# Kernel optimization log

Measured on AMD Instinct MI355X. Metric: run time of the kernel, lower is better.

Reference implementation:

```python
import jax, jax.numpy as jnp
import numpy as np

N_COARSE = 64  # n_coarse samples per ray
EPS = 1e-8
DELTA_INF = 1e10


def setup_inputs() -> dict:
    key = jax.random.key(0)
    ks = jax.random.split(key, 8)
    B, H = 16384, 256
    near = 2.0 + jax.random.uniform(ks[0], (B, 1), dtype=jnp.float32)
    far = 6.0 + jax.random.uniform(ks[1], (B, 1), dtype=jnp.float32)
    center = jax.random.normal(ks[2], (B, 3), dtype=jnp.float32)
    direction = jax.random.normal(ks[3], (B, 3), dtype=jnp.float32)
    direction = direction / jnp.linalg.norm(direction, axis=-1, keepdims=True)
    # stand-in NeRF field: 3 -> 256 -> 256 -> 4 MLP (rgb + sigma)
    W1 = jax.random.normal(ks[4], (3, H), dtype=jnp.float32) * 0.5
    b1 = jnp.zeros((H,), jnp.float32)
    W2 = jax.random.normal(ks[5], (H, H), dtype=jnp.float32) * (1.0 / np.sqrt(H))
    b2 = jnp.zeros((H,), jnp.float32)
    W3 = jax.random.normal(ks[6], (H, 4), dtype=jnp.float32) * (1.0 / np.sqrt(H))
    b3 = jnp.zeros((4,), jnp.float32)
    return {"near": near, "far": far, "center": center, "direction": direction,
            "W1": W1, "b1": b1, "W2": W2, "b2": b2, "W3": W3, "b3": b3}


def reference(near, far, center, direction, W1, b1, W2, b2, W3, b3):
    B = near.shape[0]
    K = N_COARSE
    # sample_coarse: stratified z values, lindisp=False, perturb=0
    z_steps = jnp.linspace(0.0, 1.0, K, dtype=near.dtype)[None, :]          # (1, K)
    z_vals = near * (1.0 - z_steps) + far * z_steps                          # (B, K)
    # composite(): deltas with infinite last interval
    deltas = jnp.concatenate(
        [z_vals[:, 1:] - z_vals[:, :-1],
         jnp.full((B, 1), DELTA_INF, dtype=z_vals.dtype)], axis=-1)          # (B, K)
    # world-space sample points along each ray
    points = center[:, None, :] + z_vals[:, :, None] * direction[:, None, :]  # (B, K, 3)
    # model(points) -> (B, K, 4): rgb + sigma
    h = jax.nn.relu(points @ W1 + b1)
    h = jax.nn.relu(h @ W2 + b2)
    out = h @ W3 + b3
    rgbs = out[..., :3]                                                      # (B, K, 3)
    sigmas = out[..., 3]                                                     # (B, K)
    sigmas_last = sigmas[:, -1]
    # alpha compositing (noise_std=0, training=False -> no noise)
    alphas = 1.0 - jnp.exp(-deltas * jax.nn.relu(sigmas))                    # (B, K)
    alphas_shifted = jnp.concatenate(
        [jnp.ones((B, 1), alphas.dtype), 1.0 - alphas + EPS], axis=-1)       # (B, K+1)
    T = jnp.cumprod(alphas_shifted, axis=-1)                                 # transmittance
    weights = alphas * T[:, :-1]                                             # (B, K)
    rgb_final = jnp.sum(weights[..., None] * rgbs, axis=-2)                  # (B, 3)
    depth_final = jnp.sum(weights * z_vals, axis=-1)                         # (B,)
    # white background: rgb += 1 - accumulated alpha
    pix_alpha = jnp.sum(weights, axis=1)
    rgb_final = rgb_final + 1.0 - pix_alpha[:, None]
    return rgb_final, depth_final, weights, sigmas_last
```

## Files before the change

### kernel.cpp

```cpp
#include <hip/hip_runtime.h>
#include <hip/hip_bf16.h>


constexpr int H  = 256;
constexpr int KS = 64;

typedef __attribute__((ext_vector_type(8))) short short8;
typedef __attribute__((ext_vector_type(4))) float f32x4;

__device__ __forceinline__ f32x4 mfma16(short8 a, short8 b, f32x4 c) {
    return __builtin_amdgcn_mfma_f32_16x16x32_bf16(a, b, c, 0, 0, 0);
}
__device__ __forceinline__ void split_bf16(float x, short& hi, short& lo) {
    __hip_bfloat16 h = __float2bfloat16(x);
    float hf = __bfloat162float(h);
    __hip_bfloat16 l = __float2bfloat16(x - hf);
    union { __hip_bfloat16 b; short s; } c1, c2;
    c1.b = h; c2.b = l;
    hi = c1.s; lo = c2.s;
}
__device__ __forceinline__ unsigned short f2bf(float x) {
    union { __hip_bfloat16 b; unsigned short s; } c;
    c.b = __float2bfloat16(x);
    return c.s;
}
__device__ __forceinline__ float bf2f(unsigned short s) {
    union { unsigned int u; float f; } c;
    c.u = ((unsigned int)s) << 16;
    return c.f;
}
__device__ __forceinline__ unsigned int pack2bf(float a, float b) {
    return (unsigned int)f2bf(a) | ((unsigned int)f2bf(b) << 16);
}

__global__ void pack_w2_kernel(const float* __restrict__ W2,
                               unsigned short* __restrict__ hi,
                               unsigned short* __restrict__ lo)
{
    const int i  = blockIdx.x * 256 + threadIdx.x;
    const int e  = i & 7;
    const int l  = (i >> 3) & 63;
    const int nt = (i >> 9) & 15;
    const int ks = i >> 13;
    const int k  = ks * 32 + (l >> 4) * 8 + e;
    const int n  = nt * 16 + (l & 15);
    short h, lw;
    split_bf16(W2[k * H + n], h, lw);
    hi[i] = (unsigned short)h;
    lo[i] = (unsigned short)lw;
}

struct SM {
    unsigned short A0[8 * 4 * 64 * 8];
    unsigned short A1[8 * 4 * 64 * 8];
    unsigned short L0[8 * 64 * 8];
    unsigned short L1[8 * 64 * 8];
};

#define PH1(nr_, fa_, cx_, cy_, cz_, dx_, dy_, dz_, Abuf, Lbuf)                  \
do {                                                                             \
    const int kbase = wv * 32 + (lane >> 4) * 8;                                 \
    float w1r[3][8], b1r[8];                                                     \
    _Pragma("unroll")                                                            \
    for (int c = 0; c < 3; ++c) {                                                \
        const f32x4 a_ = *(const f32x4*)&W1[c * H + kbase];                      \
        const f32x4 b_ = *(const f32x4*)&W1[c * H + kbase + 4];                  \
        _Pragma("unroll")                                                        \
        for (int e = 0; e < 4; ++e) { w1r[c][e] = a_[e]; w1r[c][e+4] = b_[e]; }  \
    }                                                                            \
    {                                                                            \
        const f32x4 a_ = *(const f32x4*)&b1[kbase];                              \
        const f32x4 b_ = *(const f32x4*)&b1[kbase + 4];                          \
        _Pragma("unroll")                                                        \
        for (int e = 0; e < 4; ++e) { b1r[e] = a_[e]; b1r[e+4] = b_[e]; }        \
    }                                                                            \
    const int prow = lane & 15;                                                  \
    _Pragma("unroll")                                                            \
    for (int mt = 0; mt < 4; ++mt) {                                             \
        const int srow = mt * 16 + prow;                                         \
        const float uu = (float)srow * (1.0f / 63.0f);                           \
        const float z  = (nr_) * (1.0f - uu) + (fa_) * uu;                       \
        const float px = (cx_) + z * (dx_), py = (cy_) + z * (dy_),              \
                    pz = (cz_) + z * (dz_);                                      \
        float xs[8];                                                             \
        _Pragma("unroll")                                                        \
        for (int e = 0; e < 8; ++e) {                                            \
            float x = fmaf(px, w1r[0][e],                                        \
                      fmaf(py, w1r[1][e],                                        \
                      fmaf(pz, w1r[2][e], b1r[e])));                             \
            xs[e] = fmaxf(x, 0.0f);                                              \
        }                                                                        \
        unsigned int hw[4];                                                      \
        _Pragma("unroll")                                                        \
        for (int p2 = 0; p2 < 4; ++p2) hw[p2] = pack2bf(xs[p2*2], xs[p2*2+1]);   \
        unsigned int* dst = (unsigned int*)&(Abuf)[((wv*4+mt)*64+lane)*8];       \
        dst[0] = hw[0]; dst[1] = hw[1]; dst[2] = hw[2]; dst[3] = hw[3];          \
        if (mt == 3) {                                                           \
            unsigned int lw[4];                                                  \
            _Pragma("unroll")                                                    \
            for (int p2 = 0; p2 < 4; ++p2) {                                     \
                const float l0 = xs[p2*2]   - bf2f((unsigned short)(hw[p2] & 0xffffu)); \
                const float l1 = xs[p2*2+1] - bf2f((unsigned short)(hw[p2] >> 16));     \
                lw[p2] = pack2bf(l0, l1);                                        \
            }                                                                    \
            unsigned int* dl = (unsigned int*)&(Lbuf)[(wv*64+lane)*8];           \
            dl[0] = lw[0]; dl[1] = lw[1]; dl[2] = lw[2]; dl[3] = lw[3];          \
        }                                                                        \
    }                                                                            \
} while (0)

#define PH2(Abuf, Lbuf, acc)                                                     \
do {                                                                             \
    const int ntg0 = wv * 2, ntg1 = ntg0 + 1;                                    \
    const short8* Bh = (const short8*)w2h;                                       \
    const short8* Bl = (const short8*)w2l;                                       \
    const short8* Ah = (const short8*)(Abuf);                                    \
    const short8* Al = (const short8*)(Lbuf);                                    \
    _Pragma("unroll 2")                                                          \
    for (int ks = 0; ks < 8; ++ks) {                                             \
        const short8 b0h  = Bh[(ks * 16 + ntg0) * 64 + lane];                    \
        const short8 b1h_ = Bh[(ks * 16 + ntg1) * 64 + lane];                    \
        _Pragma("unroll")                                                        \
        for (int mt = 0; mt < 4; ++mt) {                                         \
            const short8 ah = Ah[(ks * 4 + mt) * 64 + lane];                     \
            f32x4 c0 = acc[mt][0], c1 = acc[mt][1];                              \
            c0 = mfma16(ah, b0h, c0);                                            \
            c1 = mfma16(ah, b1h_, c1);                                           \
            if (mt == 3) {                                                       \
                const short8 b0l = Bl[(ks * 16 + ntg0) * 64 + lane];             \
                const short8 b1l = Bl[(ks * 16 + ntg1) * 64 + lane];             \
                const short8 al  = Al[ks * 64 + lane];                           \
                c0 = mfma16(ah, b0l, c0);                                        \
                c0 = mfma16(al, b0h, c0);                                        \
                c1 = mfma16(ah, b1l, c1);                                        \
                c1 = mfma16(al, b1h_, c1);                                       \
            }                                                                    \
            acc[mt][0] = c0; acc[mt][1] = c1;                                    \
        }                                                                        \
    }                                                                            \
} while (0)

#define PH3(acc, H2F, r63a_, r63b_)                                              \
do {                                                                             \
    const int rlow = (lane >> 4) * 4;                                            \
    const int hi2  = j0 >> 2;                                                    \
    const int e0   = (j0 & 3) * 2;                                               \
    _Pragma("unroll")                                                            \
    for (int mt = 0; mt < 4; ++mt) {                                             \
        const f32x4 v0 = acc[mt][0], v1 = acc[mt][1];                            \
        _Pragma("unroll")                                                        \
        for (int q = 0; q < 4; ++q) {                                            \
            const float a0 = fmaxf(v0[q], 0.0f);                                 \
            const float a1 = fmaxf(v1[q], 0.0f);                                 \
            const int l2 = (hi2 << 4) | (rlow + q);                              \
            *(unsigned int*)&(H2F)[((wv*4+mt)*64 + l2)*8 + e0] = pack2bf(a0, a1);\
            if (mt == 3 && q == 3) { r63a_ = a0; r63b_ = a1; }                   \
        }                                                                        \
    }                                                                            \
} while (0)

#define PH4(H2F, COMB, r63a_, r63b_)                                             \
do {                                                                             \
    const int hi = lane >> 4;                                                    \
    const short8* Ah2 = (const short8*)(H2F);                                    \
    _Pragma("unroll")                                                            \
    for (int mt = 0; mt < 4; ++mt) {                                             \
        const short8 a_ = Ah2[(wv * 4 + mt) * 64 + lane];                        \
        f32x4 d = (f32x4){0.f,0.f,0.f,0.f};                                      \
        d = mfma16(a_, bw3, d);                                                  \
        if (j0 < 4) {                                                            \
            _Pragma("unroll")                                                    \
            for (int q = 0; q < 4; ++q)                                          \
                (COMB)[(wv * 64 + mt * 16 + hi * 4 + q) * 4 + j0] = d[q];        \
        }                                                                        \
    }                                                                            \
    if (lastGrp) {                                                               \
        float p = fmaf(r63a_, w3A, r63b_ * w3B);                                 \
        _Pragma("unroll")                                                        \
        for (int off = 1; off < 16; off <<= 1) p += __shfl_xor(p, off, 64);      \
        if (j0 == 0) (COMB)[(wv * 64 + 63) * 4 + 3] = p;                         \
    }                                                                            \
} while (0)

#define PH5(COMB, nr_, fa_, r_)                                                  \
do {                                                                             \
    if (t < KS) {                                                                \
        const int s = t;                                                         \
        f32x4 oo = (f32x4){0.f,0.f,0.f,0.f};                                     \
        _Pragma("unroll")                                                        \
        for (int q = 0; q < 8; ++q) {                                            \
            const f32x4 c_ = *(const f32x4*)&(COMB)[(q * 64 + s) * 4];           \
            oo[0] += c_[0]; oo[1] += c_[1]; oo[2] += c_[2]; oo[3] += c_[3];      \
        }                                                                        \
        const float o0 = oo[0] + b3[0];                                          \
        const float o1 = oo[1] + b3[1];                                          \
        const float o2 = oo[2] + b3[2];                                          \
        const float sigma = oo[3] + b3[3];                                       \
        const float uu = (float)s * (1.0f / 63.0f);                              \
        const float z  = (nr_) * (1.0f - uu) + (fa_) * uu;                       \
        const float u2 = (float)(s + 1) * (1.0f / 63.0f);                        \
        const float z2 = (nr_) * (1.0f - u2) + (fa_) * u2;                       \
        const float delta = (s == 63) ? 1e10f : (z2 - z);                        \
        const float alpha = 1.0f - __expf(-delta * fmaxf(sigma, 0.0f));          \
        float P = 1.0f - alpha + 1e-8f;                                          \
        _Pragma("unroll")                                                        \
        for (int off = 1; off < 64; off <<= 1) {                                 \
            const float v_ = __shfl_up(P, off, 64);                              \
            if (s >= off) P *= v_;                                               \
        }                                                                        \
        float T = __shfl_up(P, 1, 64);                                           \
        if (s == 0) T = 1.0f;                                                    \
        const float w_ = alpha * T;                                              \
        out[(size_t)B * 4 + (size_t)(r_) * 64 + s] = w_;                         \
        float ws = w_, dep = w_ * z, q0 = w_ * o0, q1 = w_ * o1, q2 = w_ * o2;   \
        _Pragma("unroll")                                                        \
        for (int off = 32; off > 0; off >>= 1) {                                 \
            ws  += __shfl_xor(ws,  off, 64);                                     \
            dep += __shfl_xor(dep, off, 64);                                     \
            q0  += __shfl_xor(q0,  off, 64);                                     \
            q1  += __shfl_xor(q1,  off, 64);                                     \
            q2  += __shfl_xor(q2,  off, 64);                                     \
        }                                                                        \
        const float sl = __shfl(sigma, 63, 64);                                  \
        if (s == 0) {                                                            \
            out[(size_t)(r_) * 3 + 0] = q0 + 1.0f - ws;                          \
            out[(size_t)(r_) * 3 + 1] = q1 + 1.0f - ws;                          \
            out[(size_t)(r_) * 3 + 2] = q2 + 1.0f - ws;                          \
            out[(size_t)B * 3 + (r_)] = dep;                                     \
            out[(size_t)B * 68 + (r_)] = sl;                                     \
        }                                                                        \
    }                                                                            \
} while (0)

__launch_bounds__(512, 4)
__global__ void nerf_mfma_kernel(
    const float* __restrict__ g_near, const float* __restrict__ g_far,
    const float* __restrict__ g_center, const float* __restrict__ g_dir,
    const float* __restrict__ W1, const float* __restrict__ b1,
    const float* __restrict__ b2,
    const float* __restrict__ W3, const float* __restrict__ b3,
    const unsigned short* __restrict__ w2h, const unsigned short* __restrict__ w2l,
    float* __restrict__ out, int B)
{
    __shared__ __align__(16) SM sm;

    const int t    = threadIdx.x;
    const int lane = t & 63;
    const int wv   = __builtin_amdgcn_readfirstlane(t >> 6);
    const int r0   = blockIdx.x * 2;
    const int r1g  = r0 + 1;
    const int r1   = min(r1g, B - 1);

    const float nr0 = g_near[r0], fa0 = g_far[r0];
    const float nr1 = g_near[r1], fa1 = g_far[r1];
    const float c0x = g_center[r0*3+0], c0y = g_center[r0*3+1], c0z = g_center[r0*3+2];
    const float d0x = g_dir[r0*3+0],    d0y = g_dir[r0*3+1],    d0z = g_dir[r0*3+2];
    const float c1x = g_center[r1*3+0], c1y = g_center[r1*3+1], c1z = g_center[r1*3+2];
    const float d1x = g_dir[r1*3+0],    d1y = g_dir[r1*3+1],    d1z = g_dir[r1*3+2];

    const int  j0 = lane & 15;
    const int  cA = wv * 32 + j0, cB = cA + 16;
    const float b2cA = b2[cA], b2cB = b2[cB];
    const float w3A = W3[cA * 4 + 3], w3B = W3[cB * 4 + 3];
    const bool lastGrp = ((lane >> 4) == 3);

    short8 bw3;
    {
        const int hi = lane >> 4;
        #pragma unroll
        for (int e = 0; e < 8; ++e) {
            const int k = wv * 32 + (e & 1) * 16 + hi * 4 + (e >> 1);
            bw3[e] = (short)f2bf((j0 < 4) ? W3[k * 4 + j0] : 0.0f);
        }
    }

    PH1(nr0, fa0, c0x, c0y, c0z, d0x, d0y, d0z, sm.A0, sm.L0);
    __syncthreads();

    f32x4 acc0[4][2];
    #pragma unroll
    for (int mt = 0; mt < 4; ++mt) {
        acc0[mt][0] = (f32x4){b2cA, b2cA, b2cA, b2cA};
        acc0[mt][1] = (f32x4){b2cB, b2cB, b2cB, b2cB};
    }
    PH2(sm.A0, sm.L0, acc0);
    PH1(nr1, fa1, c1x, c1y, c1z, d1x, d1y, d1z, sm.A1, sm.L1);
    __syncthreads();

    float r63a0 = 0.f, r63b0 = 0.f;
    PH3(acc0, sm.A0, r63a0, r63b0);
    f32x4 acc1[4][2];
    #pragma unroll
    for (int mt = 0; mt < 4; ++mt) {
        acc1[mt][0] = (f32x4){b2cA, b2cA, b2cA, b2cA};
        acc1[mt][1] = (f32x4){b2cB, b2cB, b2cB, b2cB};
    }
    PH2(sm.A1, sm.L1, acc1);
    PH4(sm.A0, (float*)sm.L0, r63a0, r63b0);
    __syncthreads();

    {
        float r63a1 = 0.f, r63b1 = 0.f;
        PH3(acc1, sm.A1, r63a1, r63b1);
        PH4(sm.A1, (float*)sm.L1, r63a1, r63b1);
    }
    PH5((const float*)sm.L0, nr0, fa0, r0);
    __syncthreads();

    if (r1g < B) PH5((const float*)sm.L1, nr1, fa1, r1g);
}

extern "C" void kernel_launch(void* const* d_in, const int* in_sizes, int n_in,
                              void* d_out, int out_size, void* d_ws, size_t ws_size,
                              hipStream_t stream)
{
    const int B = in_sizes[0];
    if (ws_size < (size_t)(2 * 65536 * sizeof(unsigned short))) return;

    unsigned short* w2h = (unsigned short*)d_ws;
    unsigned short* w2l = w2h + 65536;

    pack_w2_kernel<<<256, 256, 0, stream>>>((const float*)d_in[6], w2h, w2l);

    const int grid = (B + 1) / 2;
    nerf_mfma_kernel<<<grid, 512, 0, stream>>>(
        (const float*)d_in[0], (const float*)d_in[1],
        (const float*)d_in[2], (const float*)d_in[3],
        (const float*)d_in[4], (const float*)d_in[5],
        (const float*)d_in[7],
        (const float*)d_in[8], (const float*)d_in[9],
        w2h, w2l,
        (float*)d_out, B);
}
```

Before: 255.5 us.

## Split block into two wave groups, each owning one ray, in a staggered pipeline

```diff
diff --git a/kernel.cpp b/kernel.cpp
--- a/kernel.cpp
+++ b/kernel.cpp
@@ -57,178 +57,208 @@
     unsigned short L1[8 * 64 * 8];
 };
 
-#define PH1(nr_, fa_, cx_, cy_, cz_, dx_, dy_, dz_, Abuf, Lbuf)                  \
-do {                                                                             \
-    const int kbase = wv * 32 + (lane >> 4) * 8;                                 \
-    float w1r[3][8], b1r[8];                                                     \
-    _Pragma("unroll")                                                            \
-    for (int c = 0; c < 3; ++c) {                                                \
-        const f32x4 a_ = *(const f32x4*)&W1[c * H + kbase];                      \
-        const f32x4 b_ = *(const f32x4*)&W1[c * H + kbase + 4];                  \
-        _Pragma("unroll")                                                        \
-        for (int e = 0; e < 4; ++e) { w1r[c][e] = a_[e]; w1r[c][e+4] = b_[e]; }  \
-    }                                                                            \
-    {                                                                            \
-        const f32x4 a_ = *(const f32x4*)&b1[kbase];                              \
-        const f32x4 b_ = *(const f32x4*)&b1[kbase + 4];                          \
-        _Pragma("unroll")                                                        \
-        for (int e = 0; e < 4; ++e) { b1r[e] = a_[e]; b1r[e+4] = b_[e]; }        \
-    }                                                                            \
-    const int prow = lane & 15;                                                  \
+#define PH1(Abuf, Lbuf)                                                          \
+do {                                                                             \
+    _Pragma("unroll")                                                            \
+    for (int ii = 0; ii < 2; ++ii) {                                             \
+        const int ksi   = gw + 4 * ii;                                           \
+        const int kbase = ksi * 32 + (lane >> 4) * 8;                            \
+        float w1r[3][8], b1r[8];                                                 \
+        _Pragma("unroll")                                                        \
+        for (int c = 0; c < 3; ++c) {                                            \
+            const f32x4 a_ = *(const f32x4*)&W1[c * H + kbase];                  \
+            const f32x4 b_ = *(const f32x4*)&W1[c * H + kbase + 4];              \
+            _Pragma("unroll")                                                    \
+            for (int e = 0; e < 4; ++e) { w1r[c][e] = a_[e]; w1r[c][e+4] = b_[e]; } \
+        }                                                                        \
+        {                                                                        \
+            const f32x4 a_ = *(const f32x4*)&b1[kbase];                          \
+            const f32x4 b_ = *(const f32x4*)&b1[kbase + 4];                      \
+            _Pragma("unroll")                                                    \
+            for (int e = 0; e < 4; ++e) { b1r[e] = a_[e]; b1r[e+4] = b_[e]; }    \
+        }                                                                        \
+        const int prow = lane & 15;                                              \
+        _Pragma("unroll")                                                        \
+        for (int mt = 0; mt < 4; ++mt) {                                         \
+            const int srow = mt * 16 + prow;                                     \
+            const float uu = (float)srow * (1.0f / 63.0f);                       \
+            const float z  = nr * (1.0f - uu) + fa * uu;                         \
+            const float px = cx + z * dx, py = cy + z * dy, pz = cz + z * dz;    \
+            float xs[8];                                                         \
+            _Pragma("unroll")                                                    \
+            for (int e = 0; e < 8; ++e) {                                        \
+                float x = fmaf(px, w1r[0][e],                                    \
+                          fmaf(py, w1r[1][e],                                    \
+                          fmaf(pz, w1r[2][e], b1r[e])));                         \
+                xs[e] = fmaxf(x, 0.0f);                                          \
+            }                                                                    \
+            unsigned int hw[4];                                                  \
+            _Pragma("unroll")                                                    \
+            for (int p2 = 0; p2 < 4; ++p2) hw[p2] = pack2bf(xs[p2*2], xs[p2*2+1]); \
+            unsigned int* dst = (unsigned int*)&(Abuf)[((ksi*4+mt)*64+lane)*8];  \
+            dst[0] = hw[0]; dst[1] = hw[1]; dst[2] = hw[2]; dst[3] = hw[3];      \
+            if (mt == 3) {                                                       \
+                unsigned int lw[4];                                              \
+                _Pragma("unroll")                                                \
+                for (int p2 = 0; p2 < 4; ++p2) {                                 \
+                    const float l0 = xs[p2*2]   - bf2f((unsigned short)(hw[p2] & 0xffffu)); \
+                    const float l1 = xs[p2*2+1] - bf2f((unsigned short)(hw[p2] >> 16));     \
+                    lw[p2] = pack2bf(l0, l1);                                    \
+                }                                                                \
+                unsigned int* dl = (unsigned int*)&(Lbuf)[(ksi*64+lane)*8];      \
+                dl[0] = lw[0]; dl[1] = lw[1]; dl[2] = lw[2]; dl[3] = lw[3];      \
+            }                                                                    \
+        }                                                                        \
+    }                                                                            \
+} while (0)
+
+#define ACCINIT()                                                                \
+do {                                                                             \
     _Pragma("unroll")                                                            \
     for (int mt = 0; mt < 4; ++mt) {                                             \
-        const int srow = mt * 16 + prow;                                         \
-        const float uu = (float)srow * (1.0f / 63.0f);                           \
-        const float z  = (nr_) * (1.0f - uu) + (fa_) * uu;                       \
-        const float px = (cx_) + z * (dx_), py = (cy_) + z * (dy_),              \
-                    pz = (cz_) + z * (dz_);                                      \
-        float xs[8];                                                             \
-        _Pragma("unroll")                                                        \
-        for (int e = 0; e < 8; ++e) {                                            \
-            float x = fmaf(px, w1r[0][e],                                        \
-                      fmaf(py, w1r[1][e],                                        \
-                      fmaf(pz, w1r[2][e], b1r[e])));                             \
-            xs[e] = fmaxf(x, 0.0f);                                              \
-        }                                                                        \
-        unsigned int hw[4];                                                      \
-        _Pragma("unroll")                                                        \
-        for (int p2 = 0; p2 < 4; ++p2) hw[p2] = pack2bf(xs[p2*2], xs[p2*2+1]);   \
-        unsigned int* dst = (unsigned int*)&(Abuf)[((wv*4+mt)*64+lane)*8];       \
-        dst[0] = hw[0]; dst[1] = hw[1]; dst[2] = hw[2]; dst[3] = hw[3];          \
-        if (mt == 3) {                                                           \
-            unsigned int lw[4];                                                  \
-            _Pragma("unroll")                                                    \
-            for (int p2 = 0; p2 < 4; ++p2) {                                     \
-                const float l0 = xs[p2*2]   - bf2f((unsigned short)(hw[p2] & 0xffffu)); \
-                const float l1 = xs[p2*2+1] - bf2f((unsigned short)(hw[p2] >> 16));     \
-                lw[p2] = pack2bf(l0, l1);                                        \
-            }                                                                    \
-            unsigned int* dl = (unsigned int*)&(Lbuf)[(wv*64+lane)*8];           \
-            dl[0] = lw[0]; dl[1] = lw[1]; dl[2] = lw[2]; dl[3] = lw[3];          \
-        }                                                                        \
-    }                                                                            \
-} while (0)
-
-#define PH2(Abuf, Lbuf, acc)                                                     \
-do {                                                                             \
-    const int ntg0 = wv * 2, ntg1 = ntg0 + 1;                                    \
+        acc[mt][0] = (f32x4){b2c0_, b2c0_, b2c0_, b2c0_};                        \
+        acc[mt][1] = (f32x4){b2c1_, b2c1_, b2c1_, b2c1_};                        \
+        acc[mt][2] = (f32x4){b2c2_, b2c2_, b2c2_, b2c2_};                        \
+        acc[mt][3] = (f32x4){b2c3_, b2c3_, b2c3_, b2c3_};                        \
+    }                                                                            \
+} while (0)
+
+#define PH2(Abuf, Lbuf)                                                          \
+do {                                                                             \
     const short8* Bh = (const short8*)w2h;                                       \
     const short8* Bl = (const short8*)w2l;                                       \
     const short8* Ah = (const short8*)(Abuf);                                    \
     const short8* Al = (const short8*)(Lbuf);                                    \
-    _Pragma("unroll 2")                                                          \
+    __builtin_amdgcn_s_setprio(1);                                               \
+    _Pragma("unroll 1")                                                          \
     for (int ks = 0; ks < 8; ++ks) {                                             \
-        const short8 b0h  = Bh[(ks * 16 + ntg0) * 64 + lane];                    \
-        const short8 b1h_ = Bh[(ks * 16 + ntg1) * 64 + lane];                    \
+        short8 bh[4];                                                            \
+        _Pragma("unroll")                                                        \
+        for (int v = 0; v < 4; ++v)                                              \
+            bh[v] = Bh[(ks * 16 + gw * 4 + v) * 64 + lane];                      \
         _Pragma("unroll")                                                        \
         for (int mt = 0; mt < 4; ++mt) {                                         \
             const short8 ah = Ah[(ks * 4 + mt) * 64 + lane];                     \
-            f32x4 c0 = acc[mt][0], c1 = acc[mt][1];                              \
-            c0 = mfma16(ah, b0h, c0);                                            \
-            c1 = mfma16(ah, b1h_, c1);                                           \
+            _Pragma("unroll")                                                    \
+            for (int v = 0; v < 4; ++v)                                          \
+                acc[mt][v] = mfma16(ah, bh[v], acc[mt][v]);                      \
             if (mt == 3) {                                                       \
-                const short8 b0l = Bl[(ks * 16 + ntg0) * 64 + lane];             \
-                const short8 b1l = Bl[(ks * 16 + ntg1) * 64 + lane];             \
-                const short8 al  = Al[ks * 64 + lane];                           \
-                c0 = mfma16(ah, b0l, c0);                                        \
-                c0 = mfma16(al, b0h, c0);                                        \
-                c1 = mfma16(ah, b1l, c1);                                        \
-                c1 = mfma16(al, b1h_, c1);                                       \
+                const short8 al = Al[ks * 64 + lane];                            \
+                _Pragma("unroll")                                                \
+                for (int v = 0; v < 4; ++v) {                                    \
+                    const short8 bl = Bl[(ks * 16 + gw * 4 + v) * 64 + lane];    \
+                    acc[3][v] = mfma16(ah, bl, acc[3][v]);                       \
+                    acc[3][v] = mfma16(al, bh[v], acc[3][v]);                    \
+                }                                                                \
             }                                                                    \
-            acc[mt][0] = c0; acc[mt][1] = c1;                                    \
-        }                                                                        \
-    }                                                                            \
-} while (0)
-
-#define PH3(acc, H2F, r63a_, r63b_)                                              \
+        }                                                                        \
+    }                                                                            \
+    __builtin_amdgcn_s_setprio(0);                                               \
+} while (0)
+
+#define PH3(H2F)                                                                 \
 do {                                                                             \
     const int rlow = (lane >> 4) * 4;                                            \
     const int hi2  = j0 >> 2;                                                    \
     const int e0   = (j0 & 3) * 2;                                               \
     _Pragma("unroll")                                                            \
     for (int mt = 0; mt < 4; ++mt) {                                             \
-        const f32x4 v0 = acc[mt][0], v1 = acc[mt][1];                            \
         _Pragma("unroll")                                                        \
         for (int q = 0; q < 4; ++q) {                                            \
-            const float a0 = fmaxf(v0[q], 0.0f);                                 \
-            const float a1 = fmaxf(v1[q], 0.0f);                                 \
+            const float a0 = fmaxf(acc[mt][0][q], 0.0f);                         \
+            const float a1 = fmaxf(acc[mt][1][q], 0.0f);                         \
+            const float a2 = fmaxf(acc[mt][2][q], 0.0f);                         \
+            const float a3 = fmaxf(acc[mt][3][q], 0.0f);                         \
             const int l2 = (hi2 << 4) | (rlow + q);                              \
-            *(unsigned int*)&(H2F)[((wv*4+mt)*64 + l2)*8 + e0] = pack2bf(a0, a1);\
-            if (mt == 3 && q == 3) { r63a_ = a0; r63b_ = a1; }                   \
-        }                                                                        \
-    }                                                                            \
-} while (0)
-
-#define PH4(H2F, COMB, r63a_, r63b_)                                             \
+            *(unsigned int*)&(H2F)[(((gw*2+0)*4+mt)*64 + l2)*8 + e0] = pack2bf(a0, a1); \
+            *(unsigned int*)&(H2F)[(((gw*2+1)*4+mt)*64 + l2)*8 + e0] = pack2bf(a2, a3); \
+            if (mt == 3 && q == 3) { r63_0 = a0; r63_1 = a1; r63_2 = a2; r63_3 = a3; } \
+        }                                                                        \
+    }                                                                            \
+} while (0)
+
+#define PH4(H2F, COMB)                                                           \
 do {                                                                             \
     const int hi = lane >> 4;                                                    \
+    short8 bw0, bw1;                                                             \
+    _Pragma("unroll")                                                            \
+    for (int e = 0; e < 8; ++e) {                                                \
+        const int kl = (e & 1) * 16 + hi * 4 + (e >> 1);                         \
+        const int k0 = 64 * gw + kl;                                             \
+        const int k1 = k0 + 32;                                                  \
+        bw0[e] = (short)f2bf((j0 < 4) ? W3[k0 * 4 + j0] : 0.0f);                 \
+        bw1[e] = (short)f2bf((j0 < 4) ? W3[k1 * 4 + j0] : 0.0f);                 \
+    }                                                                            \
     const short8* Ah2 = (const short8*)(H2F);                                    \
     _Pragma("unroll")                                                            \
     for (int mt = 0; mt < 4; ++mt) {                                             \
-        const short8 a_ = Ah2[(wv * 4 + mt) * 64 + lane];                        \
+        const short8 a0_ = Ah2[((gw*2+0)*4 + mt)*64 + lane];                     \
+        const short8 a1_ = Ah2[((gw*2+1)*4 + mt)*64 + lane];                     \
         f32x4 d = (f32x4){0.f,0.f,0.f,0.f};                                      \
-        d = mfma16(a_, bw3, d);                                                  \
+        d = mfma16(a0_, bw0, d);                                                 \
+        d = mfma16(a1_, bw1, d);                                                 \
         if (j0 < 4) {                                                            \
             _Pragma("unroll")                                                    \
             for (int q = 0; q < 4; ++q)                                          \
-                (COMB)[(wv * 64 + mt * 16 + hi * 4 + q) * 4 + j0] = d[q];        \
+                (COMB)[(gw * 64 + mt * 16 + hi * 4 + q) * 4 + j0] = d[q];        \
         }                                                                        \
     }                                                                            \
     if (lastGrp) {                                                               \
-        float p = fmaf(r63a_, w3A, r63b_ * w3B);                                 \
+        float p = fmaf(r63_0, W3[(64*gw+j0)*4+3],                                \
+                  fmaf(r63_1, W3[(64*gw+16+j0)*4+3],                             \
+                  fmaf(r63_2, W3[(64*gw+32+j0)*4+3],                             \
+                       r63_3 * W3[(64*gw+48+j0)*4+3])));                         \
         _Pragma("unroll")                                                        \
         for (int off = 1; off < 16; off <<= 1) p += __shfl_xor(p, off, 64);      \
-        if (j0 == 0) (COMB)[(wv * 64 + 63) * 4 + 3] = p;                         \
-    }                                                                            \
-} while (0)
-
-#define PH5(COMB, nr_, fa_, r_)                                                  \
-do {                                                                             \
-    if (t < KS) {                                                                \
-        const int s = t;                                                         \
-        f32x4 oo = (f32x4){0.f,0.f,0.f,0.f};                                     \
-        _Pragma("unroll")                                                        \
-        for (int q = 0; q < 8; ++q) {                                            \
-            const f32x4 c_ = *(const f32x4*)&(COMB)[(q * 64 + s) * 4];           \
-            oo[0] += c_[0]; oo[1] += c_[1]; oo[2] += c_[2]; oo[3] += c_[3];      \
-        }                                                                        \
-        const float o0 = oo[0] + b3[0];                                          \
-        const float o1 = oo[1] + b3[1];                                          \
-        const float o2 = oo[2] + b3[2];                                          \
-        const float sigma = oo[3] + b3[3];                                       \
-        const float uu = (float)s * (1.0f / 63.0f);                              \
-        const float z  = (nr_) * (1.0f - uu) + (fa_) * uu;                       \
-        const float u2 = (float)(s + 1) * (1.0f / 63.0f);                        \
-        const float z2 = (nr_) * (1.0f - u2) + (fa_) * u2;                       \
-        const float delta = (s == 63) ? 1e10f : (z2 - z);                        \
-        const float alpha = 1.0f - __expf(-delta * fmaxf(sigma, 0.0f));          \
-        float P = 1.0f - alpha + 1e-8f;                                          \
-        _Pragma("unroll")                                                        \
-        for (int off = 1; off < 64; off <<= 1) {                                 \
-            const float v_ = __shfl_up(P, off, 64);                              \
-            if (s >= off) P *= v_;                                               \
-        }                                                                        \
-        float T = __shfl_up(P, 1, 64);                                           \
-        if (s == 0) T = 1.0f;                                                    \
-        const float w_ = alpha * T;                                              \
-        out[(size_t)B * 4 + (size_t)(r_) * 64 + s] = w_;                         \
-        float ws = w_, dep = w_ * z, q0 = w_ * o0, q1 = w_ * o1, q2 = w_ * o2;   \
-        _Pragma("unroll")                                                        \
-        for (int off = 32; off > 0; off >>= 1) {                                 \
-            ws  += __shfl_xor(ws,  off, 64);                                     \
-            dep += __shfl_xor(dep, off, 64);                                     \
-            q0  += __shfl_xor(q0,  off, 64);                                     \
-            q1  += __shfl_xor(q1,  off, 64);                                     \
-            q2  += __shfl_xor(q2,  off, 64);                                     \
-        }                                                                        \
-        const float sl = __shfl(sigma, 63, 64);                                  \
-        if (s == 0) {                                                            \
-            out[(size_t)(r_) * 3 + 0] = q0 + 1.0f - ws;                          \
-            out[(size_t)(r_) * 3 + 1] = q1 + 1.0f - ws;                          \
-            out[(size_t)(r_) * 3 + 2] = q2 + 1.0f - ws;                          \
-            out[(size_t)B * 3 + (r_)] = dep;                                     \
-            out[(size_t)B * 68 + (r_)] = sl;                                     \
-        }                                                                        \
+        if (j0 == 0) (COMB)[(gw * 64 + 63) * 4 + 3] = p;                         \
+    }                                                                            \
+} while (0)
+
+#define PH5(COMB, r_)                                                            \
+do {                                                                             \
+    const int s = lane;                                                          \
+    f32x4 oo = (f32x4){0.f,0.f,0.f,0.f};                                         \
+    _Pragma("unroll")                                                            \
+    for (int q = 0; q < 4; ++q) {                                                \
+        const f32x4 c_ = *(const f32x4*)&(COMB)[(q * 64 + s) * 4];               \
+        oo[0] += c_[0]; oo[1] += c_[1]; oo[2] += c_[2]; oo[3] += c_[3];          \
+    }                                                                            \
+    const float o0 = oo[0] + b3[0];                                              \
+    const float o1 = oo[1] + b3[1];                                              \
+    const float o2 = oo[2] + b3[2];                                              \
+    const float sigma = oo[3] + b3[3];                                           \
+    const float uu = (float)s * (1.0f / 63.0f);                                  \
+    const float z  = nr * (1.0f - uu) + fa * uu;                                 \
+    const float u2 = (float)(s + 1) * (1.0f / 63.0f);                            \
+    const float z2 = nr * (1.0f - u2) + fa * u2;                                 \
+    const float delta = (s == 63) ? 1e10f : (z2 - z);                            \
+    const float alpha = 1.0f - __expf(-delta * fmaxf(sigma, 0.0f));              \
+    float P = 1.0f - alpha + 1e-8f;                                              \
+    _Pragma("unroll")                                                            \
+    for (int off = 1; off < 64; off <<= 1) {                                     \
+        const float v_ = __shfl_up(P, off, 64);                                  \
+        if (s >= off) P *= v_;                                                   \
+    }                                                                            \
+    float T = __shfl_up(P, 1, 64);                                               \
+    if (s == 0) T = 1.0f;                                                        \
+    const float w_ = alpha * T;                                                  \
+    out[(size_t)B * 4 + (size_t)(r_) * 64 + s] = w_;                             \
+    float ws = w_, dep = w_ * z, q0 = w_ * o0, q1 = w_ * o1, q2 = w_ * o2;       \
+    _Pragma("unroll")                                                            \
+    for (int off = 32; off > 0; off >>= 1) {                                     \
+        ws  += __shfl_xor(ws,  off, 64);                                         \
+        dep += __shfl_xor(dep, off, 64);                                         \
+        q0  += __shfl_xor(q0,  off, 64);                                         \
+        q1  += __shfl_xor(q1,  off, 64);                                         \
+        q2  += __shfl_xor(q2,  off, 64);                                         \
+    }                                                                            \
+    const float sl = __shfl(sigma, 63, 64);                                      \
+    if (s == 0) {                                                                \
+        out[(size_t)(r_) * 3 + 0] = q0 + 1.0f - ws;                              \
+        out[(size_t)(r_) * 3 + 1] = q1 + 1.0f - ws;                              \
+        out[(size_t)(r_) * 3 + 2] = q2 + 1.0f - ws;                              \
+        out[(size_t)B * 3 + (r_)] = dep;                                         \
+        out[(size_t)B * 68 + (r_)] = sl;                                         \
     }                                                                            \
 } while (0)
 
@@ -247,67 +277,47 @@
     const int t    = threadIdx.x;
     const int lane = t & 63;
     const int wv   = __builtin_amdgcn_readfirstlane(t >> 6);
+    const int grp  = wv >> 2;
+    const int gw   = wv & 3;
     const int r0   = blockIdx.x * 2;
     const int r1g  = r0 + 1;
-    const int r1   = min(r1g, B - 1);
-
-    const float nr0 = g_near[r0], fa0 = g_far[r0];
-    const float nr1 = g_near[r1], fa1 = g_far[r1];
-    const float c0x = g_center[r0*3+0], c0y = g_center[r0*3+1], c0z = g_center[r0*3+2];
-    const float d0x = g_dir[r0*3+0],    d0y = g_dir[r0*3+1],    d0z = g_dir[r0*3+2];
-    const float c1x = g_center[r1*3+0], c1y = g_center[r1*3+1], c1z = g_center[r1*3+2];
-    const float d1x = g_dir[r1*3+0],    d1y = g_dir[r1*3+1],    d1z = g_dir[r1*3+2];
+    const int ray  = grp ? min(r1g, B - 1) : r0;
+    const int rOut = grp ? r1g : r0;
+
+    const float nr = g_near[ray], fa = g_far[ray];
+    const float cx = g_center[ray*3+0], cy = g_center[ray*3+1], cz = g_center[ray*3+2];
+    const float dx = g_dir[ray*3+0],    dy = g_dir[ray*3+1],    dz = g_dir[ray*3+2];
 
     const int  j0 = lane & 15;
-    const int  cA = wv * 32 + j0, cB = cA + 16;
-    const float b2cA = b2[cA], b2cB = b2[cB];
-    const float w3A = W3[cA * 4 + 3], w3B = W3[cB * 4 + 3];
     const bool lastGrp = ((lane >> 4) == 3);
-
-    short8 bw3;
-    {
-        const int hi = lane >> 4;
-        #pragma unroll
-        for (int e = 0; e < 8; ++e) {
-            const int k = wv * 32 + (e & 1) * 16 + hi * 4 + (e >> 1);
-            bw3[e] = (short)f2bf((j0 < 4) ? W3[k * 4 + j0] : 0.0f);
-        }
-    }
-
-    PH1(nr0, fa0, c0x, c0y, c0z, d0x, d0y, d0z, sm.A0, sm.L0);
+    const float b2c0_ = b2[64*gw + j0];
+    const float b2c1_ = b2[64*gw + 16 + j0];
+    const float b2c2_ = b2[64*gw + 32 + j0];
+    const float b2c3_ = b2[64*gw + 48 + j0];
+
+    unsigned short* Abuf = grp ? sm.A1 : sm.A0;
+    unsigned short* Lbuf = grp ? sm.L1 : sm.L0;
+    float* COMB = (float*)Lbuf;
+
+    f32x4 acc[4][4];
+    float r63_0 = 0.f, r63_1 = 0.f, r63_2 = 0.f, r63_3 = 0.f;
+
+    if (!grp) PH1(Abuf, Lbuf);
     __syncthreads();
 
-    f32x4 acc0[4][2];
-    #pragma unroll
-    for (int mt = 0; mt < 4; ++mt) {
-        acc0[mt][0] = (f32x4){b2cA, b2cA, b2cA, b2cA};
-        acc0[mt][1] = (f32x4){b2cB, b2cB, b2cB, b2cB};
-    }
-    PH2(sm.A0, sm.L0, acc0);
-    PH1(nr1, fa1, c1x, c1y, c1z, d1x, d1y, d1z, sm.A1, sm.L1);
+    if (!grp) { ACCINIT(); PH2(Abuf, Lbuf); }
+    else      { PH1(Abuf, Lbuf); }
     __syncthreads();
 
-    float r63a0 = 0.f, r63b0 = 0.f;
-    PH3(acc0, sm.A0, r63a0, r63b0);
-    f32x4 acc1[4][2];
-    #pragma unroll
-    for (int mt = 0; mt < 4; ++mt) {
-        acc1[mt][0] = (f32x4){b2cA, b2cA, b2cA, b2cA};
-        acc1[mt][1] = (f32x4){b2cB, b2cB, b2cB, b2cB};
-    }
-    PH2(sm.A1, sm.L1, acc1);
-    PH4(sm.A0, (float*)sm.L0, r63a0, r63b0);
+    if (!grp) { PH3(Abuf); PH4(Abuf, COMB); }
+    else      { ACCINIT(); PH2(Abuf, Lbuf); }
     __syncthreads();
 
-    {
-        float r63a1 = 0.f, r63b1 = 0.f;
-        PH3(acc1, sm.A1, r63a1, r63b1);
-        PH4(sm.A1, (float*)sm.L1, r63a1, r63b1);
-    }
-    PH5((const float*)sm.L0, nr0, fa0, r0);
+    if (!grp) { if (gw == 0) PH5(COMB, r0); }
+    else      { PH3(Abuf); PH4(Abuf, COMB); }
     __syncthreads();
 
-    if (r1g < B) PH5((const float*)sm.L1, nr1, fa1, r1g);
+    if (grp && gw == 0 && rOut < B) PH5(COMB, rOut);
 }
 
 extern "C" void kernel_launch(void* const* d_in, const int* in_sizes, int n_in,
```

Result: slower. 265.2 us (+3.8%).
